# Optimization experiments

Measured on AMD Instinct MI355X. Metric: run time of the kernel, lower is better.

## Reference

```python
import jax, jax.numpy as jnp
import numpy as np

KH, KW = 7, 7
H, W = 4096, 4096

def setup_inputs() -> dict:
    key = jax.random.key(0)
    k1, k2 = jax.random.split(key)
    x = jax.random.normal(k1, (H, W), dtype=jnp.float32)
    weight = jax.random.normal(k2, (KH, KW), dtype=jnp.float32) * 0.001
    bias = jnp.zeros((1,), dtype=jnp.float32)
    return {"x": x, "weight": weight, "bias": bias}

def reference(x, weight, bias):
    # Single-channel valid 2D cross-correlation + scalar bias.
    # lax.conv_general_dilated performs cross-correlation (no kernel flip),
    # matching the torch loop: res[i,j] = sum(x[i:i+kh, j:j+kw] * k).
    lhs = x[None, None, :, :]            # [N=1, C=1, H, W]
    rhs = weight[None, None, :, :]       # [O=1, I=1, kh, kw]
    out = jax.lax.conv_general_dilated(
        lhs, rhs,
        window_strides=(1, 1),
        padding="VALID",
        dimension_numbers=("NCHW", "OIHW", "NCHW"),
    )
    return out[0, 0] + bias[0]           # [H-kh+1, W-kw+1]
```

## Files before the change

### kernel.cpp

```cpp
#include <hip/hip_runtime.h>

#define IH 4096
#define IW 4096
#define KH 7
#define KW 7
#define OH 4090
#define OW 4090

#define TW 256
#define TH 16
#define LW 272
#define LH (TH + 6)
#define NV4 (LW / 4)
#define NLD (LH * NV4)

typedef float v2f __attribute__((ext_vector_type(2)));

__global__ __launch_bounds__(256) void conv7x7_kernel(
    const float* __restrict__ x,
    const float* __restrict__ w,
    const float* __restrict__ bias,
    float* __restrict__ out)
{
    __shared__ float smem[LH * LW];

    const int tid     = threadIdx.x;
    const int tile_x0 = blockIdx.x * TW;
    const int tile_y0 = blockIdx.y * TH;

    float wt[KH * KW];
#pragma unroll
    for (int k = 0; k < KH * KW; ++k) wt[k] = w[k];
    const float b = bias[0];

#pragma unroll
    for (int i = 0; i < (NLD + 255) / 256; ++i) {
        const int f = tid + i * 256;
        if (f < NLD) {
            const int r  = f / NV4;
            const int c4 = f - r * NV4;
            int iy = tile_y0 + r;
            iy = iy < IH ? iy : IH - 1;
            const float* xr = x + (size_t)iy * IW;
            const int c0 = tile_x0 + 4 * c4;
            float4 v;
            if (c0 + 3 < IW) {
                v = *(const float4*)(xr + c0);
            } else {
                const int j0 = c0     < IW ? c0     : IW - 1;
                const int j1 = c0 + 1 < IW ? c0 + 1 : IW - 1;
                const int j2 = c0 + 2 < IW ? c0 + 2 : IW - 1;
                const int j3 = c0 + 3 < IW ? c0 + 3 : IW - 1;
                v = make_float4(xr[j0], xr[j1], xr[j2], xr[j3]);
            }
            *(float4*)(&smem[r * LW + 4 * c4]) = v;
        }
    }
    __syncthreads();

    const int tx  = tid & 63;
    const int ty  = tid >> 6;
    const int lx0 = 4 * tx;

    float acc[4][4];
#pragma unroll
    for (int r = 0; r < 4; ++r)
#pragma unroll
        for (int c = 0; c < 4; ++c) acc[r][c] = b;

#pragma unroll
    for (int ir = 0; ir < TH / 4 * 0 + 10; ++ir) {
        const float* srow = &smem[(4 * ty + ir) * LW + lx0];
        float rbuf[10];
        const float4 q0 = *(const float4*)(srow);
        const float4 q1 = *(const float4*)(srow + 4);
        const float2 q2 = *(const float2*)(srow + 8);
        rbuf[0]=q0.x; rbuf[1]=q0.y; rbuf[2]=q0.z; rbuf[3]=q0.w;
        rbuf[4]=q1.x; rbuf[5]=q1.y; rbuf[6]=q1.z; rbuf[7]=q1.w;
        rbuf[8]=q2.x; rbuf[9]=q2.y;

#pragma unroll
        for (int ky = 0; ky < KH; ++ky) {
            const int ry = ir - ky;
            if (ry >= 0 && ry < 4) {
#pragma unroll
                for (int kx = 0; kx < KW; ++kx) {
                    const float wv = wt[ky * KW + kx];
#pragma unroll
                    for (int c = 0; c < 4; ++c)
                        acc[ry][c] += wv * rbuf[kx + c];
                }
            }
        }
    }

    const int ox0 = tile_x0 + lx0;
#pragma unroll
    for (int ry = 0; ry < 4; ++ry) {
        const int oy = tile_y0 + 4 * ty + ry;
        if (oy < OH) {
            float* orow = out + (size_t)oy * OW;
            if (ox0 + 3 < OW) {
                v2f v0 = { acc[ry][0], acc[ry][1] };
                v2f v1 = { acc[ry][2], acc[ry][3] };
                __builtin_nontemporal_store(v0, (v2f*)(orow + ox0));
                __builtin_nontemporal_store(v1, (v2f*)(orow + ox0 + 2));
            } else {
#pragma unroll
                for (int c = 0; c < 4; ++c)
                    if (ox0 + c < OW) orow[ox0 + c] = acc[ry][c];
            }
        }
    }
}

extern "C" void kernel_launch(void* const* d_in, const int* in_sizes, int n_in,
                              void* d_out, int out_size, void* d_ws, size_t ws_size,
                              hipStream_t stream) {
    const float* x    = (const float*)d_in[0];
    const float* w    = (const float*)d_in[1];
    const float* bias = (const float*)d_in[2];
    float* out        = (float*)d_out;

    dim3 grid((OW + TW - 1) / TW, (OH + TH - 1) / TH);
    conv7x7_kernel<<<grid, dim3(256), 0, stream>>>(x, w, bias, out);
}
```

Baseline: 144.3 us.

## Double-buffer input tiles with async global-to-LDS loads across row steps

Each block now handles four vertical 16-row tiles in sequence instead of one. It keeps two LDS buffers and issues the next tile's load with the direct global-to-LDS load builtin, so that load runs while the current tile is being computed. This aims to hide global load latency and skip the register round trip when staging the halo tile. In exchange the grid is four times smaller, which cuts the number of blocks available to hide latency, and LDS use per block doubles.

After: 130.2 us. -9.8%, faster.

```diff
diff --git a/kernel.cpp b/kernel.cpp
--- a/kernel.cpp
+++ b/kernel.cpp
@@ -1,38 +1,28 @@
 #include <hip/hip_runtime.h>
+#include <stdint.h>
 
 #define IH 4096
 #define IW 4096
-#define KH 7
-#define KW 7
 #define OH 4090
 #define OW 4090
 
 #define TW 256
 #define TH 16
 #define LW 272
-#define LH (TH + 6)
-#define NV4 (LW / 4)
+#define LH 22
+#define NV4 68
 #define NLD (LH * NV4)
+#define STEPS 4
 
 typedef float v2f __attribute__((ext_vector_type(2)));
+typedef __attribute__((address_space(1))) void gas_void;
+typedef __attribute__((address_space(3))) void las_void;
 
-__global__ __launch_bounds__(256) void conv7x7_kernel(
-    const float* __restrict__ x,
-    const float* __restrict__ w,
-    const float* __restrict__ bias,
-    float* __restrict__ out)
+__device__ __forceinline__ void stage_tile(const float* __restrict__ x,
+                                           int tile_y0, int tile_x0,
+                                           float* sbuf, int tid)
 {
-    __shared__ float smem[LH * LW];
-
-    const int tid     = threadIdx.x;
-    const int tile_x0 = blockIdx.x * TW;
-    const int tile_y0 = blockIdx.y * TH;
-
-    float wt[KH * KW];
-#pragma unroll
-    for (int k = 0; k < KH * KW; ++k) wt[k] = w[k];
-    const float b = bias[0];
-
+    const int wv = tid >> 6;
 #pragma unroll
     for (int i = 0; i < (NLD + 255) / 256; ++i) {
         const int f = tid + i * 256;
@@ -41,74 +31,94 @@
             const int c4 = f - r * NV4;
             int iy = tile_y0 + r;
             iy = iy < IH ? iy : IH - 1;
-            const float* xr = x + (size_t)iy * IW;
-            const int c0 = tile_x0 + 4 * c4;
-            float4 v;
-            if (c0 + 3 < IW) {
-                v = *(const float4*)(xr + c0);
-            } else {
-                const int j0 = c0     < IW ? c0     : IW - 1;
-                const int j1 = c0 + 1 < IW ? c0 + 1 : IW - 1;
-                const int j2 = c0 + 2 < IW ? c0 + 2 : IW - 1;
-                const int j3 = c0 + 3 < IW ? c0 + 3 : IW - 1;
-                v = make_float4(xr[j0], xr[j1], xr[j2], xr[j3]);
-            }
-            *(float4*)(&smem[r * LW + 4 * c4]) = v;
+            int c0 = tile_x0 + 4 * c4;
+            c0 = c0 <= IW - 4 ? c0 : IW - 4;
+            const float* gp = x + (size_t)iy * IW + c0;
+            float* lp = sbuf + (size_t)(i * 256 + wv * 64) * 4;
+            __builtin_amdgcn_global_load_lds((gas_void*)gp, (las_void*)lp, 16, 0, 0);
         }
     }
-    __syncthreads();
+}
+
+__global__ __launch_bounds__(256) void conv7x7_kernel(
+    const float* __restrict__ x,
+    const float* __restrict__ w,
+    const float* __restrict__ bias,
+    float* __restrict__ out)
+{
+    __shared__ float smem[2][LH * LW];
+
+    const int tid     = threadIdx.x;
+    const int tile_x0 = blockIdx.x * TW;
+    const int ytile0  = blockIdx.y * STEPS;
+
+    float wt[49];
+#pragma unroll
+    for (int k = 0; k < 49; ++k) wt[k] = w[k];
+    const float b = bias[0];
+
+    stage_tile(x, ytile0 * TH, tile_x0, smem[0], tid);
 
     const int tx  = tid & 63;
-    const int ty  = tid >> 6;
+    const int wv  = tid >> 6;
     const int lx0 = 4 * tx;
 
-    float acc[4][4];
+    for (int s = 0; s < STEPS; ++s) {
+        __syncthreads();
+        if (s + 1 < STEPS)
+            stage_tile(x, (ytile0 + s + 1) * TH, tile_x0, smem[(s + 1) & 1], tid);
+
+        const float* sb = smem[s & 1];
+
+        float acc[4][4];
 #pragma unroll
-    for (int r = 0; r < 4; ++r)
+        for (int r = 0; r < 4; ++r)
 #pragma unroll
-        for (int c = 0; c < 4; ++c) acc[r][c] = b;
+            for (int c = 0; c < 4; ++c) acc[r][c] = b;
 
 #pragma unroll
-    for (int ir = 0; ir < TH / 4 * 0 + 10; ++ir) {
-        const float* srow = &smem[(4 * ty + ir) * LW + lx0];
-        float rbuf[10];
-        const float4 q0 = *(const float4*)(srow);
-        const float4 q1 = *(const float4*)(srow + 4);
-        const float2 q2 = *(const float2*)(srow + 8);
-        rbuf[0]=q0.x; rbuf[1]=q0.y; rbuf[2]=q0.z; rbuf[3]=q0.w;
-        rbuf[4]=q1.x; rbuf[5]=q1.y; rbuf[6]=q1.z; rbuf[7]=q1.w;
-        rbuf[8]=q2.x; rbuf[9]=q2.y;
+        for (int ir = 0; ir < 10; ++ir) {
+            const float* srow = sb + (4 * wv + ir) * LW + lx0;
+            const float4 q0 = *(const float4*)(srow);
+            const float4 q1 = *(const float4*)(srow + 4);
+            const float4 q2 = *(const float4*)(srow + 8);
+            float rb[12];
+            rb[0]=q0.x; rb[1]=q0.y; rb[2]=q0.z;  rb[3]=q0.w;
+            rb[4]=q1.x; rb[5]=q1.y; rb[6]=q1.z;  rb[7]=q1.w;
+            rb[8]=q2.x; rb[9]=q2.y; rb[10]=q2.z; rb[11]=q2.w;
 
 #pragma unroll
-        for (int ky = 0; ky < KH; ++ky) {
-            const int ry = ir - ky;
-            if (ry >= 0 && ry < 4) {
+            for (int ky = 0; ky < 7; ++ky) {
+                const int ry = ir - ky;
+                if (ry >= 0 && ry < 4) {
 #pragma unroll
-                for (int kx = 0; kx < KW; ++kx) {
-                    const float wv = wt[ky * KW + kx];
+                    for (int kx = 0; kx < 7; ++kx) {
+                        const float wv_ = wt[ky * 7 + kx];
 #pragma unroll
-                    for (int c = 0; c < 4; ++c)
-                        acc[ry][c] += wv * rbuf[kx + c];
+                        for (int c = 0; c < 4; ++c)
+                            acc[ry][c] += wv_ * rb[kx + c];
+                    }
                 }
             }
         }
-    }
 
-    const int ox0 = tile_x0 + lx0;
+        const int ox0 = tile_x0 + lx0;
+        const int oyb = (ytile0 + s) * TH + 4 * wv;
 #pragma unroll
-    for (int ry = 0; ry < 4; ++ry) {
-        const int oy = tile_y0 + 4 * ty + ry;
-        if (oy < OH) {
-            float* orow = out + (size_t)oy * OW;
-            if (ox0 + 3 < OW) {
-                v2f v0 = { acc[ry][0], acc[ry][1] };
-                v2f v1 = { acc[ry][2], acc[ry][3] };
-                __builtin_nontemporal_store(v0, (v2f*)(orow + ox0));
-                __builtin_nontemporal_store(v1, (v2f*)(orow + ox0 + 2));
-            } else {
+        for (int ry = 0; ry < 4; ++ry) {
+            const int oy = oyb + ry;
+            if (oy < OH) {
+                float* orow = out + (size_t)oy * OW;
+                if (ox0 + 3 < OW) {
+                    v2f v0 = { acc[ry][0], acc[ry][1] };
+                    v2f v1 = { acc[ry][2], acc[ry][3] };
+                    __builtin_nontemporal_store(v0, (v2f*)(orow + ox0));
+                    __builtin_nontemporal_store(v1, (v2f*)(orow + ox0 + 2));
+                } else {
 #pragma unroll
-                for (int c = 0; c < 4; ++c)
-                    if (ox0 + c < OW) orow[ox0 + c] = acc[ry][c];
+                    for (int c = 0; c < 4; ++c)
+                        if (ox0 + c < OW) orow[ox0 + c] = acc[ry][c];
+                }
             }
         }
     }
@@ -122,6 +132,6 @@
     const float* bias = (const float*)d_in[2];
     float* out        = (float*)d_out;
 
-    dim3 grid((OW + TW - 1) / TW, (OH + TH - 1) / TH);
+    dim3 grid((OW + TW - 1) / TW, (4096 / TH) / STEPS);
     conv7x7_kernel<<<grid, dim3(256), 0, stream>>>(x, w, bias, out);
 }
```
